# Kernel optimization log

Hardware: AMD Instinct MI355X
Metric: run time of the kernel (lower is better)

Reference implementation:

```python
import jax, jax.numpy as jnp
import numpy as np

D_MODEL = 1024
N_HEADS = 16
D_HEAD = D_MODEL // N_HEADS
SCALE = 1.0 / np.sqrt(D_HEAD)


def setup_inputs() -> dict:
    key = jax.random.key(0)
    ks = jax.random.split(key, 5)
    B, S = 2, 2048
    x = jax.random.normal(ks[0], (B, S, D_MODEL), dtype=jnp.float32)
    # torch F.linear weights have shape (d_out, d_in); kaiming-uniform-ish init
    bound = 1.0 / np.sqrt(D_MODEL)
    Wq = jax.random.uniform(ks[1], (D_MODEL, D_MODEL), jnp.float32, -bound, bound)
    Wk = jax.random.uniform(ks[2], (D_MODEL, D_MODEL), jnp.float32, -bound, bound)
    Wv = jax.random.uniform(ks[3], (D_MODEL, D_MODEL), jnp.float32, -bound, bound)
    Wo = jax.random.uniform(ks[4], (D_MODEL, D_MODEL), jnp.float32, -bound, bound)
    return {"x": x, "Wq": Wq, "Wk": Wk, "Wv": Wv, "Wo": Wo}


def reference(x, Wq, Wk, Wv, Wo):
    B, S, _ = x.shape
    # F.linear(x, W) = x @ W.T; reshape to [B, H, S, Dh]
    def proj(W):
        return (x @ W.T).reshape(B, S, N_HEADS, D_HEAD).transpose(0, 2, 1, 3)
    Q, K, V = proj(Wq), proj(Wk), proj(Wv)
    # scores [B, H, S, S]
    attn = jnp.einsum('bhqd,bhkd->bhqk', Q, K) * SCALE
    causal = jnp.tril(jnp.ones((S, S), dtype=bool))
    attn = jnp.where(causal, attn, -jnp.inf)
    attn = jax.nn.softmax(attn, axis=-1)
    out = jnp.einsum('bhqk,bhkd->bhqd', attn, V)
    out = out.transpose(0, 2, 1, 3).reshape(B, S, D_MODEL)
    return out @ Wo.T
```

## Files before the change

kernel.cpp:

```cpp
#include <hip/hip_runtime.h>


typedef __attribute__((ext_vector_type(8))) short short8;
typedef __attribute__((ext_vector_type(4))) float f32x4;
typedef __attribute__((ext_vector_type(4))) _Float16 half4;

#if __has_builtin(__builtin_amdgcn_exp2f)
#define EXP2F(x) __builtin_amdgcn_exp2f(x)
#else
#define EXP2F(x) exp2f(x)
#endif

__device__ __forceinline__ unsigned short f2bf(float f) {
  unsigned int x = __float_as_uint(f);
  x += 0x7fffu + ((x >> 16) & 1u);
  return (unsigned short)(x >> 16);
}

__device__ __forceinline__ void gload16(const void* g, void* l) {
  __builtin_amdgcn_global_load_lds(
      (const __attribute__((address_space(1))) void*)g,
      (__attribute__((address_space(3))) void*)l, 16, 0, 0);
}

__device__ __forceinline__ int swz64(int row, int sc) {
  return row * 64 + ((((sc >> 3) ^ (row & 7)) << 3) | (sc & 7));
}

__device__ __forceinline__ int swzG(int row, int chunk) {
  return row * 32 + (((chunk ^ ((row >> 1) & 3)) << 3));
}

__global__ void cast_kernel(const float* __restrict__ x, const float* __restrict__ wq,
                            const float* __restrict__ wk, const float* __restrict__ wv,
                            const float* __restrict__ wo,
                            unsigned short* __restrict__ xb, unsigned short* __restrict__ wqb,
                            unsigned short* __restrict__ wkb, unsigned short* __restrict__ wvb,
                            unsigned short* __restrict__ wob) {
  int id = blockIdx.x;
  const float* in; unsigned short* out; int blk; float sc = 1.f;
  if (id < 4096) { in = x; out = xb; blk = id; }
  else {
    int wsel = (id - 4096) >> 10;
    blk = (id - 4096) & 1023;
    switch (wsel) {
      case 0: in = wq; out = wqb; sc = 0.18033688011112042f; break;
      case 1: in = wk; out = wkb; break;
      case 2: in = wv; out = wvb; break;
      default: in = wo; out = wob; break;
    }
  }
  int i = blk * 256 + threadIdx.x;
  float4 v = ((const float4*)in)[i];
  union { unsigned short u[4]; uint2 p; } o;
  o.u[0] = f2bf(v.x * sc); o.u[1] = f2bf(v.y * sc);
  o.u[2] = f2bf(v.z * sc); o.u[3] = f2bf(v.w * sc);
  ((uint2*)out)[i] = o.p;
}

#define GK 1024

__global__ __launch_bounds__(256) void gemm_qkv_kernel(
    const unsigned short* __restrict__ X,
    const unsigned short* __restrict__ Wq,
    const unsigned short* __restrict__ Wk,
    const unsigned short* __restrict__ Wv,
    unsigned short* __restrict__ Qo,
    unsigned short* __restrict__ Ko,
    _Float16* __restrict__ Vt) {
  __shared__ unsigned short As[2][128 * 32];
  __shared__ unsigned short Bs[2][128 * 32];
  int id = blockIdx.x;
  int xcd = id & 7, j = id >> 3;
  int mb = j / 3;
  int nbT = xcd * 3 + (j - mb * 3);
  int sel = nbT >> 3, nb = nbT & 7;
  const unsigned short* W = sel == 0 ? Wq : (sel == 1 ? Wk : Wv);

  int tid = threadIdx.x;
  int w = tid >> 6, l = tid & 63, quad = l >> 4, lo = l & 15;
  int wm = (w >> 1) * 64, wn = (w & 1) * 64;

  int srow = tid >> 2;
  int slc = (tid & 3) ^ ((srow >> 1) & 3);
  int srow2 = (256 + tid) >> 2;
  int slc2 = (tid & 3) ^ ((srow2 >> 1) & 3);

  f32x4 acc[4][4];
#pragma unroll
  for (int i = 0; i < 4; i++)
#pragma unroll
    for (int jj = 0; jj < 4; jj++) acc[i][jj] = (f32x4){0.f, 0.f, 0.f, 0.f};

  gload16(X + (size_t)(mb * 128 + srow) * GK + slc * 8, (char*)As[0] + tid * 16);
  gload16(W + (size_t)(nb * 128 + srow) * GK + slc * 8, (char*)Bs[0] + tid * 16);
  gload16(X + (size_t)(mb * 128 + srow2) * GK + slc2 * 8, (char*)As[0] + (256 + tid) * 16);
  gload16(W + (size_t)(nb * 128 + srow2) * GK + slc2 * 8, (char*)Bs[0] + (256 + tid) * 16);

  for (int kt = 0; kt < 32; kt++) {
    __syncthreads();
    if (kt + 1 < 32) {
      int nb_ = (kt + 1) & 1, k0 = (kt + 1) * 32;
      gload16(X + (size_t)(mb * 128 + srow) * GK + k0 + slc * 8, (char*)As[nb_] + tid * 16);
      gload16(W + (size_t)(nb * 128 + srow) * GK + k0 + slc * 8, (char*)Bs[nb_] + tid * 16);
      gload16(X + (size_t)(mb * 128 + srow2) * GK + k0 + slc2 * 8,
              (char*)As[nb_] + (256 + tid) * 16);
      gload16(W + (size_t)(nb * 128 + srow2) * GK + k0 + slc2 * 8,
              (char*)Bs[nb_] + (256 + tid) * 16);
    }
    const unsigned short* as = As[kt & 1];
    const unsigned short* bs = Bs[kt & 1];
    short8 a[4], b[4];
#pragma unroll
    for (int mi = 0; mi < 4; mi++)
      a[mi] = *(const short8*)&as[swzG(wm + mi * 16 + lo, quad)];
#pragma unroll
    for (int ni = 0; ni < 4; ni++)
      b[ni] = *(const short8*)&bs[swzG(wn + ni * 16 + lo, quad)];
#pragma unroll
    for (int mi = 0; mi < 4; mi++)
#pragma unroll
      for (int ni = 0; ni < 4; ni++)
        acc[mi][ni] = __builtin_amdgcn_mfma_f32_16x16x32_bf16(a[mi], b[ni],
                                                              acc[mi][ni], 0, 0, 0);
  }
  if (sel == 2) {
#pragma unroll
    for (int mi = 0; mi < 4; mi++)
#pragma unroll
      for (int ni = 0; ni < 4; ni++) {
        int row0 = mb * 128 + wm + mi * 16 + quad * 4;
        int col = nb * 128 + wn + ni * 16 + lo;
        int bb = row0 >> 11, ss = row0 & 2047;
        int hh = col >> 6, dd = col & 63;
        half4 v;
#pragma unroll
        for (int r = 0; r < 4; r++) v[r] = (_Float16)acc[mi][ni][r];
        *(half4*)&Vt[((size_t)((bb * 16 + hh) * 64 + dd)) * 2048 + ss] = v;
      }
  } else {
    unsigned short* C = sel == 0 ? Qo : Ko;
#pragma unroll
    for (int mi = 0; mi < 4; mi++)
#pragma unroll
      for (int ni = 0; ni < 4; ni++)
#pragma unroll
        for (int r = 0; r < 4; r++) {
          int row = mb * 128 + wm + mi * 16 + quad * 4 + r;
          int col = nb * 128 + wn + ni * 16 + lo;
          C[(size_t)row * 1024 + col] = f2bf(acc[mi][ni][r]);
        }
  }
}

__global__ __launch_bounds__(256) void gemm_out_kernel(
    const unsigned short* __restrict__ A,
    const unsigned short* __restrict__ W,
    float* __restrict__ C) {
  __shared__ unsigned short As[2][128 * 32];
  __shared__ unsigned short Bs[2][64 * 32];
  int id = blockIdx.x;
  int nb = ((id & 7) << 1) | ((id >> 3) & 1);
  int mb = id >> 4;
  int tid = threadIdx.x;
  int w = tid >> 6, l = tid & 63, quad = l >> 4, lo = l & 15;
  int wm = w * 32;

  int srow = tid >> 2;
  int slc = (tid & 3) ^ ((srow >> 1) & 3);
  int srow2 = (256 + tid) >> 2;
  int slc2 = (tid & 3) ^ ((srow2 >> 1) & 3);

  f32x4 acc[2][4];
#pragma unroll
  for (int i = 0; i < 2; i++)
#pragma unroll
    for (int jj = 0; jj < 4; jj++) acc[i][jj] = (f32x4){0.f, 0.f, 0.f, 0.f};

  gload16(A + (size_t)(mb * 128 + srow) * GK + slc * 8, (char*)As[0] + tid * 16);
  gload16(A + (size_t)(mb * 128 + srow2) * GK + slc2 * 8, (char*)As[0] + (256 + tid) * 16);
  gload16(W + (size_t)(nb * 64 + srow) * GK + slc * 8, (char*)Bs[0] + tid * 16);

  for (int kt = 0; kt < 32; kt++) {
    __syncthreads();
    if (kt + 1 < 32) {
      int nb_ = (kt + 1) & 1, k0 = (kt + 1) * 32;
      gload16(A + (size_t)(mb * 128 + srow) * GK + k0 + slc * 8, (char*)As[nb_] + tid * 16);
      gload16(A + (size_t)(mb * 128 + srow2) * GK + k0 + slc2 * 8,
              (char*)As[nb_] + (256 + tid) * 16);
      gload16(W + (size_t)(nb * 64 + srow) * GK + k0 + slc * 8, (char*)Bs[nb_] + tid * 16);
    }
    const unsigned short* as = As[kt & 1];
    const unsigned short* bs = Bs[kt & 1];
    short8 a[2], b[4];
#pragma unroll
    for (int mi = 0; mi < 2; mi++)
      a[mi] = *(const short8*)&as[swzG(wm + mi * 16 + lo, quad)];
#pragma unroll
    for (int ni = 0; ni < 4; ni++)
      b[ni] = *(const short8*)&bs[swzG(ni * 16 + lo, quad)];
#pragma unroll
    for (int mi = 0; mi < 2; mi++)
#pragma unroll
      for (int ni = 0; ni < 4; ni++)
        acc[mi][ni] = __builtin_amdgcn_mfma_f32_16x16x32_bf16(a[mi], b[ni],
                                                              acc[mi][ni], 0, 0, 0);
  }
#pragma unroll
  for (int mi = 0; mi < 2; mi++)
#pragma unroll
    for (int ni = 0; ni < 4; ni++)
#pragma unroll
      for (int r = 0; r < 4; r++) {
        int row = mb * 128 + wm + mi * 16 + quad * 4 + r;
        int col = nb * 64 + ni * 16 + lo;
        C[(size_t)row * 1024 + col] = acc[mi][ni][r];
      }
}

__global__ __launch_bounds__(256, 4) void attn_kernel(
    const unsigned short* __restrict__ Q,
    const unsigned short* __restrict__ K,
    const _Float16* __restrict__ Vt,
    unsigned short* __restrict__ O) {
  const int S = 2048, DM = 1024;
  __shared__ unsigned short Ks[2][64 * 64];
  __shared__ _Float16 Vts[2][64 * 64];

  int id = blockIdx.x;
  int bh = ((id & 7) << 2) | ((id >> 3) & 3);
  int qt = 31 - (id >> 5);
  int b = bh >> 4, h = bh & 15;
  size_t base = (size_t)b * S * DM + h * 64;
  size_t baseVt = (size_t)(bh * 64) * S;

  int tid = threadIdx.x;
  int w = tid >> 6, lane = tid & 63, quad = lane >> 4, lo = lane & 15;
  int qrow0 = qt * 64 + w * 16;
  const half4 ones = {(_Float16)1.f, (_Float16)1.f, (_Float16)1.f, (_Float16)1.f};

  short8 qf[2];
#pragma unroll
  for (int d = 0; d < 2; d++)
    qf[d] = *(const short8*)(Q + base + (size_t)(qrow0 + lo) * DM + d * 32 + quad * 8);

#pragma unroll
  for (int jj = 0; jj < 2; jj++) {
    int s_ = jj * 256 + tid;
    int row = s_ >> 3, lc = (s_ & 7) ^ (row & 7);
    gload16(K + base + (size_t)row * DM + lc * 8, (char*)Ks[0] + s_ * 16);
    gload16(Vt + baseVt + (size_t)row * S + lc * 8, (char*)Vts[0] + s_ * 16);
  }

  f32x4 oacc[4], lacc;
  lacc = (f32x4){0.f, 0.f, 0.f, 0.f};
#pragma unroll
  for (int ni = 0; ni < 4; ni++) oacc[ni] = (f32x4){0.f, 0.f, 0.f, 0.f};

  int tend = qt + 1;
  for (int t = 0; t < tend; t++) {
    __syncthreads();
    if (t + 1 < tend) {
      int tb = (t + 1) & 1;
#pragma unroll
      for (int jj = 0; jj < 2; jj++) {
        int s_ = jj * 256 + tid;
        int row = s_ >> 3, lc = (s_ & 7) ^ (row & 7);
        gload16(K + base + (size_t)((t + 1) * 64 + row) * DM + lc * 8,
                (char*)Ks[tb] + s_ * 16);
        gload16(Vt + baseVt + (size_t)row * S + (t + 1) * 64 + lc * 8,
                (char*)Vts[tb] + s_ * 16);
      }
    }
    const unsigned short* ks = Ks[t & 1];
    const _Float16* vs = Vts[t & 1];

    f32x4 st[4];
#pragma unroll
    for (int kvt = 0; kvt < 4; kvt++) st[kvt] = (f32x4){0.f, 0.f, 0.f, 0.f};
#pragma unroll
    for (int kvt = 0; kvt < 4; kvt++)
#pragma unroll
      for (int d = 0; d < 2; d++) {
        short8 kf = *(const short8*)&ks[swz64(kvt * 16 + lo, d * 32 + quad * 8)];
        st[kvt] = __builtin_amdgcn_mfma_f32_16x16x32_bf16(kf, qf[d], st[kvt], 0, 0, 0);
      }

    if (t == tend - 1) {
      int qg = qrow0 + lo;
#pragma unroll
      for (int kvt = 0; kvt < 4; kvt++)
#pragma unroll
        for (int r = 0; r < 4; r++) {
          int kv = t * 64 + kvt * 16 + quad * 4 + r;
          if (kv > qg) st[kvt][r] = -1e30f;
        }
    }

    half4 pf[4];
#pragma unroll
    for (int kvt = 0; kvt < 4; kvt++) {
      half4 p4;
#pragma unroll
      for (int r = 0; r < 4; r++) p4[r] = (_Float16)EXP2F(st[kvt][r]);
      pf[kvt] = p4;
    }

#pragma unroll
    for (int kvt = 0; kvt < 4; kvt++) {
#pragma unroll
      for (int ni = 0; ni < 4; ni++) {
        half4 vf = *(const half4*)&vs[swz64(ni * 16 + lo, kvt * 16 + quad * 4)];
        oacc[ni] = __builtin_amdgcn_mfma_f32_16x16x16f16(pf[kvt], vf, oacc[ni], 0, 0, 0);
      }
      lacc = __builtin_amdgcn_mfma_f32_16x16x16f16(pf[kvt], ones, lacc, 0, 0, 0);
    }
  }

  float inv[4];
#pragma unroll
  for (int r = 0; r < 4; r++) inv[r] = 1.0f / lacc[r];
#pragma unroll
  for (int ni = 0; ni < 4; ni++)
#pragma unroll
    for (int r = 0; r < 4; r++) {
      int qg = qrow0 + quad * 4 + r;
      O[base + (size_t)qg * DM + ni * 16 + lo] = f2bf(oacc[ni][r] * inv[r]);
    }
}

extern "C" void kernel_launch(void* const* d_in, const int* in_sizes, int n_in,
                              void* d_out, int out_size, void* d_ws, size_t ws_size,
                              hipStream_t stream) {
  const float* x  = (const float*)d_in[0];
  const float* Wq = (const float*)d_in[1];
  const float* Wk = (const float*)d_in[2];
  const float* Wv = (const float*)d_in[3];
  const float* Wo = (const float*)d_in[4];
  float* out = (float*)d_out;
  char* ws = (char*)d_ws;

  unsigned short* Xb  = (unsigned short*)(ws);
  unsigned short* Wqb = (unsigned short*)(ws + (8ll  << 20));
  unsigned short* Wkb = (unsigned short*)(ws + (10ll << 20));
  unsigned short* Wvb = (unsigned short*)(ws + (12ll << 20));
  unsigned short* Wob = (unsigned short*)(ws + (14ll << 20));
  unsigned short* Qb  = (unsigned short*)(ws + (16ll << 20));
  unsigned short* Kb  = (unsigned short*)(ws + (24ll << 20));
  _Float16*       Vt  = (_Float16*)     (ws + (32ll << 20));
  unsigned short* Ob  = (unsigned short*)(ws + (40ll << 20));

  cast_kernel<<<8192, 256, 0, stream>>>(x, Wq, Wk, Wv, Wo, Xb, Wqb, Wkb, Wvb, Wob);
  gemm_qkv_kernel<<<768, 256, 0, stream>>>(Xb, Wqb, Wkb, Wvb, Qb, Kb, Vt);
  attn_kernel<<<1024, 256, 0, stream>>>(Qb, Kb, Vt, Ob);
  gemm_out_kernel<<<512, 256, 0, stream>>>(Ob, Wob, out);
}
```

Measured before the change: 182.1 us.

## Fuse all four stages into one persistent cooperative kernel with grid syncs

```diff
diff --git a/kernel.cpp b/kernel.cpp
--- a/kernel.cpp
+++ b/kernel.cpp
@@ -1,4 +1,7 @@
 #include <hip/hip_runtime.h>
+#include <hip/hip_cooperative_groups.h>
+
+namespace cg = cooperative_groups;
 
 
 typedef __attribute__((ext_vector_type(8))) short short8;
@@ -31,302 +34,294 @@
   return row * 32 + (((chunk ^ ((row >> 1) & 3)) << 3));
 }
 
-__global__ void cast_kernel(const float* __restrict__ x, const float* __restrict__ wq,
-                            const float* __restrict__ wk, const float* __restrict__ wv,
-                            const float* __restrict__ wo,
-                            unsigned short* __restrict__ xb, unsigned short* __restrict__ wqb,
-                            unsigned short* __restrict__ wkb, unsigned short* __restrict__ wvb,
-                            unsigned short* __restrict__ wob) {
-  int id = blockIdx.x;
-  const float* in; unsigned short* out; int blk; float sc = 1.f;
-  if (id < 4096) { in = x; out = xb; blk = id; }
-  else {
-    int wsel = (id - 4096) >> 10;
-    blk = (id - 4096) & 1023;
-    switch (wsel) {
-      case 0: in = wq; out = wqb; sc = 0.18033688011112042f; break;
-      case 1: in = wk; out = wkb; break;
-      case 2: in = wv; out = wvb; break;
-      default: in = wo; out = wob; break;
+__global__ __launch_bounds__(256, 3) void fused_kernel(
+    const float* __restrict__ x, const float* __restrict__ wq,
+    const float* __restrict__ wk, const float* __restrict__ wv,
+    const float* __restrict__ wo,
+    unsigned short* __restrict__ Xb, unsigned short* __restrict__ Wqb,
+    unsigned short* __restrict__ Wkb, unsigned short* __restrict__ Wvb,
+    unsigned short* __restrict__ Wob,
+    unsigned short* __restrict__ Qb, unsigned short* __restrict__ Kb,
+    _Float16* __restrict__ Vt, unsigned short* __restrict__ Ob,
+    float* __restrict__ out, int* __restrict__ ctr) {
+  cg::grid_group grid = cg::this_grid();
+  __shared__ __attribute__((aligned(16))) char smem[32768];
+  __shared__ int t_sh;
+  const int G = gridDim.x;
+  const int id = blockIdx.x, tid = threadIdx.x;
+  const int w = tid >> 6, lane = tid & 63, quad = lane >> 4, lo = lane & 15;
+  const int S = 2048, DM = 1024;
+
+  if (id == 0 && tid == 0) ctr[0] = 0;
+  for (long long j = (long long)id * 256 + tid; j < 2097152; j += (long long)G * 256) {
+    const float* in; unsigned short* outp; long long off; float sc = 1.f;
+    if (j < 1048576) { in = x; outp = Xb; off = j; }
+    else {
+      int wsel = (int)((j - 1048576) >> 18);
+      off = (j - 1048576) & 262143;
+      switch (wsel) {
+        case 0: in = wq; outp = Wqb; sc = 0.18033688011112042f; break;
+        case 1: in = wk; outp = Wkb; break;
+        case 2: in = wv; outp = Wvb; break;
+        default: in = wo; outp = Wob; break;
+      }
+    }
+    float4 v = ((const float4*)in)[off];
+    union { unsigned short u[4]; uint2 p; } o;
+    o.u[0] = f2bf(v.x * sc); o.u[1] = f2bf(v.y * sc);
+    o.u[2] = f2bf(v.z * sc); o.u[3] = f2bf(v.w * sc);
+    ((uint2*)outp)[off] = o.p;
+  }
+  __threadfence();
+  grid.sync();
+
+  {
+    unsigned short* As = (unsigned short*)smem;
+    unsigned short* Bs = (unsigned short*)(smem + 16384);
+    const int srow = tid >> 2, slc = (tid & 3) ^ ((srow >> 1) & 3);
+    const int srow2 = (256 + tid) >> 2, slc2 = (tid & 3) ^ ((srow2 >> 1) & 3);
+    const int wm = (w >> 1) * 64, wn = (w & 1) * 64;
+    for (int tile = id; tile < 768; tile += G) {
+      const int mb = tile & 31, nbT = tile >> 5;
+      const int sel = nbT >> 3, nb = nbT & 7;
+      const unsigned short* W = sel == 0 ? Wqb : (sel == 1 ? Wkb : Wvb);
+      const unsigned short* Xa  = Xb + (size_t)(mb * 128 + srow ) * 1024 + slc  * 8;
+      const unsigned short* Wa  = W  + (size_t)(nb * 128 + srow ) * 1024 + slc  * 8;
+      const unsigned short* Xa2 = Xb + (size_t)(mb * 128 + srow2) * 1024 + slc2 * 8;
+      const unsigned short* Wa2 = W  + (size_t)(nb * 128 + srow2) * 1024 + slc2 * 8;
+      __syncthreads();
+      gload16(Xa,  (char*)As + tid * 16);
+      gload16(Wa,  (char*)Bs + tid * 16);
+      gload16(Xa2, (char*)As + (256 + tid) * 16);
+      gload16(Wa2, (char*)Bs + (256 + tid) * 16);
+      f32x4 acc[4][4];
+#pragma unroll
+      for (int i = 0; i < 4; i++)
+#pragma unroll
+        for (int jj = 0; jj < 4; jj++) acc[i][jj] = (f32x4){0.f, 0.f, 0.f, 0.f};
+      for (int kt = 0; kt < 32; kt++) {
+        __syncthreads();
+        if (kt + 1 < 32) {
+          const int bo = ((kt + 1) & 1) * 4096, k0 = (kt + 1) * 32;
+          gload16(Xa + k0,  (char*)(As + bo) + tid * 16);
+          gload16(Wa + k0,  (char*)(Bs + bo) + tid * 16);
+          gload16(Xa2 + k0, (char*)(As + bo) + (256 + tid) * 16);
+          gload16(Wa2 + k0, (char*)(Bs + bo) + (256 + tid) * 16);
+        }
+        const unsigned short* as = As + (kt & 1) * 4096;
+        const unsigned short* bs = Bs + (kt & 1) * 4096;
+        short8 a[4], b[4];
+#pragma unroll
+        for (int mi = 0; mi < 4; mi++)
+          a[mi] = *(const short8*)&as[swzG(wm + mi * 16 + lo, quad)];
+#pragma unroll
+        for (int ni = 0; ni < 4; ni++)
+          b[ni] = *(const short8*)&bs[swzG(wn + ni * 16 + lo, quad)];
+#pragma unroll
+        for (int mi = 0; mi < 4; mi++)
+#pragma unroll
+          for (int ni = 0; ni < 4; ni++)
+            acc[mi][ni] = __builtin_amdgcn_mfma_f32_16x16x32_bf16(a[mi], b[ni],
+                                                                  acc[mi][ni], 0, 0, 0);
+      }
+      if (sel == 2) {
+#pragma unroll
+        for (int mi = 0; mi < 4; mi++)
+#pragma unroll
+          for (int ni = 0; ni < 4; ni++) {
+            int row0 = mb * 128 + wm + mi * 16 + quad * 4;
+            int col = nb * 128 + wn + ni * 16 + lo;
+            int bb = row0 >> 11, ss = row0 & 2047;
+            int hh = col >> 6, dd = col & 63;
+            half4 v;
+#pragma unroll
+            for (int r = 0; r < 4; r++) v[r] = (_Float16)acc[mi][ni][r];
+            *(half4*)&Vt[((size_t)((bb * 16 + hh) * 64 + dd)) * 2048 + ss] = v;
+          }
+      } else {
+        unsigned short* C = sel == 0 ? Qb : Kb;
+#pragma unroll
+        for (int mi = 0; mi < 4; mi++)
+#pragma unroll
+          for (int ni = 0; ni < 4; ni++)
+#pragma unroll
+            for (int r = 0; r < 4; r++) {
+              int row = mb * 128 + wm + mi * 16 + quad * 4 + r;
+              int col = nb * 128 + wn + ni * 16 + lo;
+              C[(size_t)row * 1024 + col] = f2bf(acc[mi][ni][r]);
+            }
+      }
     }
   }
-  int i = blk * 256 + threadIdx.x;
-  float4 v = ((const float4*)in)[i];
-  union { unsigned short u[4]; uint2 p; } o;
-  o.u[0] = f2bf(v.x * sc); o.u[1] = f2bf(v.y * sc);
-  o.u[2] = f2bf(v.z * sc); o.u[3] = f2bf(v.w * sc);
-  ((uint2*)out)[i] = o.p;
-}
-
-#define GK 1024
-
-__global__ __launch_bounds__(256) void gemm_qkv_kernel(
-    const unsigned short* __restrict__ X,
-    const unsigned short* __restrict__ Wq,
-    const unsigned short* __restrict__ Wk,
-    const unsigned short* __restrict__ Wv,
-    unsigned short* __restrict__ Qo,
-    unsigned short* __restrict__ Ko,
-    _Float16* __restrict__ Vt) {
-  __shared__ unsigned short As[2][128 * 32];
-  __shared__ unsigned short Bs[2][128 * 32];
-  int id = blockIdx.x;
-  int xcd = id & 7, j = id >> 3;
-  int mb = j / 3;
-  int nbT = xcd * 3 + (j - mb * 3);
-  int sel = nbT >> 3, nb = nbT & 7;
-  const unsigned short* W = sel == 0 ? Wq : (sel == 1 ? Wk : Wv);
-
-  int tid = threadIdx.x;
-  int w = tid >> 6, l = tid & 63, quad = l >> 4, lo = l & 15;
-  int wm = (w >> 1) * 64, wn = (w & 1) * 64;
-
-  int srow = tid >> 2;
-  int slc = (tid & 3) ^ ((srow >> 1) & 3);
-  int srow2 = (256 + tid) >> 2;
-  int slc2 = (tid & 3) ^ ((srow2 >> 1) & 3);
-
-  f32x4 acc[4][4];
-#pragma unroll
-  for (int i = 0; i < 4; i++)
-#pragma unroll
-    for (int jj = 0; jj < 4; jj++) acc[i][jj] = (f32x4){0.f, 0.f, 0.f, 0.f};
-
-  gload16(X + (size_t)(mb * 128 + srow) * GK + slc * 8, (char*)As[0] + tid * 16);
-  gload16(W + (size_t)(nb * 128 + srow) * GK + slc * 8, (char*)Bs[0] + tid * 16);
-  gload16(X + (size_t)(mb * 128 + srow2) * GK + slc2 * 8, (char*)As[0] + (256 + tid) * 16);
-  gload16(W + (size_t)(nb * 128 + srow2) * GK + slc2 * 8, (char*)Bs[0] + (256 + tid) * 16);
-
-  for (int kt = 0; kt < 32; kt++) {
-    __syncthreads();
-    if (kt + 1 < 32) {
-      int nb_ = (kt + 1) & 1, k0 = (kt + 1) * 32;
-      gload16(X + (size_t)(mb * 128 + srow) * GK + k0 + slc * 8, (char*)As[nb_] + tid * 16);
-      gload16(W + (size_t)(nb * 128 + srow) * GK + k0 + slc * 8, (char*)Bs[nb_] + tid * 16);
-      gload16(X + (size_t)(mb * 128 + srow2) * GK + k0 + slc2 * 8,
-              (char*)As[nb_] + (256 + tid) * 16);
-      gload16(W + (size_t)(nb * 128 + srow2) * GK + k0 + slc2 * 8,
-              (char*)Bs[nb_] + (256 + tid) * 16);
-    }
-    const unsigned short* as = As[kt & 1];
-    const unsigned short* bs = Bs[kt & 1];
-    short8 a[4], b[4];
-#pragma unroll
-    for (int mi = 0; mi < 4; mi++)
-      a[mi] = *(const short8*)&as[swzG(wm + mi * 16 + lo, quad)];
-#pragma unroll
-    for (int ni = 0; ni < 4; ni++)
-      b[ni] = *(const short8*)&bs[swzG(wn + ni * 16 + lo, quad)];
-#pragma unroll
-    for (int mi = 0; mi < 4; mi++)
-#pragma unroll
-      for (int ni = 0; ni < 4; ni++)
-        acc[mi][ni] = __builtin_amdgcn_mfma_f32_16x16x32_bf16(a[mi], b[ni],
-                                                              acc[mi][ni], 0, 0, 0);
-  }
-  if (sel == 2) {
-#pragma unroll
-    for (int mi = 0; mi < 4; mi++)
-#pragma unroll
-      for (int ni = 0; ni < 4; ni++) {
-        int row0 = mb * 128 + wm + mi * 16 + quad * 4;
-        int col = nb * 128 + wn + ni * 16 + lo;
-        int bb = row0 >> 11, ss = row0 & 2047;
-        int hh = col >> 6, dd = col & 63;
-        half4 v;
-#pragma unroll
-        for (int r = 0; r < 4; r++) v[r] = (_Float16)acc[mi][ni][r];
-        *(half4*)&Vt[((size_t)((bb * 16 + hh) * 64 + dd)) * 2048 + ss] = v;
-      }
-  } else {
-    unsigned short* C = sel == 0 ? Qo : Ko;
-#pragma unroll
-    for (int mi = 0; mi < 4; mi++)
-#pragma unroll
-      for (int ni = 0; ni < 4; ni++)
-#pragma unroll
-        for (int r = 0; r < 4; r++) {
-          int row = mb * 128 + wm + mi * 16 + quad * 4 + r;
-          int col = nb * 128 + wn + ni * 16 + lo;
-          C[(size_t)row * 1024 + col] = f2bf(acc[mi][ni][r]);
-        }
-  }
-}
-
-__global__ __launch_bounds__(256) void gemm_out_kernel(
-    const unsigned short* __restrict__ A,
-    const unsigned short* __restrict__ W,
-    float* __restrict__ C) {
-  __shared__ unsigned short As[2][128 * 32];
-  __shared__ unsigned short Bs[2][64 * 32];
-  int id = blockIdx.x;
-  int nb = ((id & 7) << 1) | ((id >> 3) & 1);
-  int mb = id >> 4;
-  int tid = threadIdx.x;
-  int w = tid >> 6, l = tid & 63, quad = l >> 4, lo = l & 15;
-  int wm = w * 32;
-
-  int srow = tid >> 2;
-  int slc = (tid & 3) ^ ((srow >> 1) & 3);
-  int srow2 = (256 + tid) >> 2;
-  int slc2 = (tid & 3) ^ ((srow2 >> 1) & 3);
-
-  f32x4 acc[2][4];
-#pragma unroll
-  for (int i = 0; i < 2; i++)
-#pragma unroll
-    for (int jj = 0; jj < 4; jj++) acc[i][jj] = (f32x4){0.f, 0.f, 0.f, 0.f};
-
-  gload16(A + (size_t)(mb * 128 + srow) * GK + slc * 8, (char*)As[0] + tid * 16);
-  gload16(A + (size_t)(mb * 128 + srow2) * GK + slc2 * 8, (char*)As[0] + (256 + tid) * 16);
-  gload16(W + (size_t)(nb * 64 + srow) * GK + slc * 8, (char*)Bs[0] + tid * 16);
-
-  for (int kt = 0; kt < 32; kt++) {
-    __syncthreads();
-    if (kt + 1 < 32) {
-      int nb_ = (kt + 1) & 1, k0 = (kt + 1) * 32;
-      gload16(A + (size_t)(mb * 128 + srow) * GK + k0 + slc * 8, (char*)As[nb_] + tid * 16);
-      gload16(A + (size_t)(mb * 128 + srow2) * GK + k0 + slc2 * 8,
-              (char*)As[nb_] + (256 + tid) * 16);
-      gload16(W + (size_t)(nb * 64 + srow) * GK + k0 + slc * 8, (char*)Bs[nb_] + tid * 16);
-    }
-    const unsigned short* as = As[kt & 1];
-    const unsigned short* bs = Bs[kt & 1];
-    short8 a[2], b[4];
-#pragma unroll
-    for (int mi = 0; mi < 2; mi++)
-      a[mi] = *(const short8*)&as[swzG(wm + mi * 16 + lo, quad)];
-#pragma unroll
-    for (int ni = 0; ni < 4; ni++)
-      b[ni] = *(const short8*)&bs[swzG(ni * 16 + lo, quad)];
-#pragma unroll
-    for (int mi = 0; mi < 2; mi++)
-#pragma unroll
-      for (int ni = 0; ni < 4; ni++)
-        acc[mi][ni] = __builtin_amdgcn_mfma_f32_16x16x32_bf16(a[mi], b[ni],
-                                                              acc[mi][ni], 0, 0, 0);
-  }
-#pragma unroll
-  for (int mi = 0; mi < 2; mi++)
-#pragma unroll
-    for (int ni = 0; ni < 4; ni++)
-#pragma unroll
-      for (int r = 0; r < 4; r++) {
-        int row = mb * 128 + wm + mi * 16 + quad * 4 + r;
-        int col = nb * 64 + ni * 16 + lo;
-        C[(size_t)row * 1024 + col] = acc[mi][ni][r];
-      }
-}
-
-__global__ __launch_bounds__(256, 4) void attn_kernel(
-    const unsigned short* __restrict__ Q,
-    const unsigned short* __restrict__ K,
-    const _Float16* __restrict__ Vt,
-    unsigned short* __restrict__ O) {
-  const int S = 2048, DM = 1024;
-  __shared__ unsigned short Ks[2][64 * 64];
-  __shared__ _Float16 Vts[2][64 * 64];
-
-  int id = blockIdx.x;
-  int bh = ((id & 7) << 2) | ((id >> 3) & 3);
-  int qt = 31 - (id >> 5);
-  int b = bh >> 4, h = bh & 15;
-  size_t base = (size_t)b * S * DM + h * 64;
-  size_t baseVt = (size_t)(bh * 64) * S;
-
-  int tid = threadIdx.x;
-  int w = tid >> 6, lane = tid & 63, quad = lane >> 4, lo = lane & 15;
-  int qrow0 = qt * 64 + w * 16;
-  const half4 ones = {(_Float16)1.f, (_Float16)1.f, (_Float16)1.f, (_Float16)1.f};
-
-  short8 qf[2];
-#pragma unroll
-  for (int d = 0; d < 2; d++)
-    qf[d] = *(const short8*)(Q + base + (size_t)(qrow0 + lo) * DM + d * 32 + quad * 8);
-
-#pragma unroll
-  for (int jj = 0; jj < 2; jj++) {
-    int s_ = jj * 256 + tid;
-    int row = s_ >> 3, lc = (s_ & 7) ^ (row & 7);
-    gload16(K + base + (size_t)row * DM + lc * 8, (char*)Ks[0] + s_ * 16);
-    gload16(Vt + baseVt + (size_t)row * S + lc * 8, (char*)Vts[0] + s_ * 16);
-  }
-
-  f32x4 oacc[4], lacc;
-  lacc = (f32x4){0.f, 0.f, 0.f, 0.f};
-#pragma unroll
-  for (int ni = 0; ni < 4; ni++) oacc[ni] = (f32x4){0.f, 0.f, 0.f, 0.f};
-
-  int tend = qt + 1;
-  for (int t = 0; t < tend; t++) {
-    __syncthreads();
-    if (t + 1 < tend) {
-      int tb = (t + 1) & 1;
+  __threadfence();
+  grid.sync();
+
+  {
+    unsigned short* Ks = (unsigned short*)smem;
+    _Float16* Vts = (_Float16*)(smem + 16384);
+    const half4 ones = {(_Float16)1.f, (_Float16)1.f, (_Float16)1.f, (_Float16)1.f};
+    while (true) {
+      __syncthreads();
+      if (tid == 0) t_sh = atomicAdd(ctr, 1);
+      __syncthreads();
+      const int tk = t_sh;
+      if (tk >= 1024) break;
+      const int qt = 31 - (tk >> 5), bh = tk & 31;
+      const int b = bh >> 4, h = bh & 15;
+      const size_t base = (size_t)b * S * DM + h * 64;
+      const size_t baseVt = (size_t)(bh * 64) * S;
+      const int qrow0 = qt * 64 + w * 16;
+
+      short8 qf[2];
+#pragma unroll
+      for (int d = 0; d < 2; d++)
+        qf[d] = *(const short8*)(Qb + base + (size_t)(qrow0 + lo) * DM + d * 32 + quad * 8);
+
 #pragma unroll
       for (int jj = 0; jj < 2; jj++) {
         int s_ = jj * 256 + tid;
         int row = s_ >> 3, lc = (s_ & 7) ^ (row & 7);
-        gload16(K + base + (size_t)((t + 1) * 64 + row) * DM + lc * 8,
-                (char*)Ks[tb] + s_ * 16);
-        gload16(Vt + baseVt + (size_t)row * S + (t + 1) * 64 + lc * 8,
-                (char*)Vts[tb] + s_ * 16);
-      }
-    }
-    const unsigned short* ks = Ks[t & 1];
-    const _Float16* vs = Vts[t & 1];
-
-    f32x4 st[4];
-#pragma unroll
-    for (int kvt = 0; kvt < 4; kvt++) st[kvt] = (f32x4){0.f, 0.f, 0.f, 0.f};
-#pragma unroll
-    for (int kvt = 0; kvt < 4; kvt++)
-#pragma unroll
-      for (int d = 0; d < 2; d++) {
-        short8 kf = *(const short8*)&ks[swz64(kvt * 16 + lo, d * 32 + quad * 8)];
-        st[kvt] = __builtin_amdgcn_mfma_f32_16x16x32_bf16(kf, qf[d], st[kvt], 0, 0, 0);
-      }
-
-    if (t == tend - 1) {
-      int qg = qrow0 + lo;
-#pragma unroll
-      for (int kvt = 0; kvt < 4; kvt++)
+        gload16(Kb + base + (size_t)row * DM + lc * 8, (char*)Ks + s_ * 16);
+        gload16(Vt + baseVt + (size_t)row * S + lc * 8, (char*)Vts + s_ * 16);
+      }
+
+      f32x4 oacc[4], lacc;
+      lacc = (f32x4){0.f, 0.f, 0.f, 0.f};
+#pragma unroll
+      for (int ni = 0; ni < 4; ni++) oacc[ni] = (f32x4){0.f, 0.f, 0.f, 0.f};
+
+      const int tend = qt + 1;
+      for (int tt = 0; tt < tend; tt++) {
+        __syncthreads();
+        if (tt + 1 < tend) {
+          const int tb = ((tt + 1) & 1) * 4096;
+#pragma unroll
+          for (int jj = 0; jj < 2; jj++) {
+            int s_ = jj * 256 + tid;
+            int row = s_ >> 3, lc = (s_ & 7) ^ (row & 7);
+            gload16(Kb + base + (size_t)((tt + 1) * 64 + row) * DM + lc * 8,
+                    (char*)(Ks + tb) + s_ * 16);
+            gload16(Vt + baseVt + (size_t)row * S + (tt + 1) * 64 + lc * 8,
+                    (char*)(Vts + tb) + s_ * 16);
+          }
+        }
+        const unsigned short* ks = Ks + (tt & 1) * 4096;
+        const _Float16* vs = Vts + (tt & 1) * 4096;
+
+        f32x4 st[4];
+#pragma unroll
+        for (int kvt = 0; kvt < 4; kvt++) st[kvt] = (f32x4){0.f, 0.f, 0.f, 0.f};
+#pragma unroll
+        for (int kvt = 0; kvt < 4; kvt++)
+#pragma unroll
+          for (int d = 0; d < 2; d++) {
+            short8 kf = *(const short8*)&ks[swz64(kvt * 16 + lo, d * 32 + quad * 8)];
+            st[kvt] = __builtin_amdgcn_mfma_f32_16x16x32_bf16(kf, qf[d], st[kvt], 0, 0, 0);
+          }
+
+        if (tt == tend - 1) {
+          int qg = qrow0 + lo;
+#pragma unroll
+          for (int kvt = 0; kvt < 4; kvt++)
+#pragma unroll
+            for (int r = 0; r < 4; r++) {
+              int kv = tt * 64 + kvt * 16 + quad * 4 + r;
+              if (kv > qg) st[kvt][r] = -1e30f;
+            }
+        }
+
+        half4 pf[4];
+#pragma unroll
+        for (int kvt = 0; kvt < 4; kvt++) {
+          half4 p4;
+#pragma unroll
+          for (int r = 0; r < 4; r++) p4[r] = (_Float16)EXP2F(st[kvt][r]);
+          pf[kvt] = p4;
+        }
+
+#pragma unroll
+        for (int kvt = 0; kvt < 4; kvt++) {
+#pragma unroll
+          for (int ni = 0; ni < 4; ni++) {
+            half4 vf = *(const half4*)&vs[swz64(ni * 16 + lo, kvt * 16 + quad * 4)];
+            oacc[ni] = __builtin_amdgcn_mfma_f32_16x16x16f16(pf[kvt], vf, oacc[ni], 0, 0, 0);
+          }
+          lacc = __builtin_amdgcn_mfma_f32_16x16x16f16(pf[kvt], ones, lacc, 0, 0, 0);
+        }
+      }
+
+      float inv[4];
+#pragma unroll
+      for (int r = 0; r < 4; r++) inv[r] = 1.0f / lacc[r];
+#pragma unroll
+      for (int ni = 0; ni < 4; ni++)
 #pragma unroll
         for (int r = 0; r < 4; r++) {
-          int kv = t * 64 + kvt * 16 + quad * 4 + r;
-          if (kv > qg) st[kvt][r] = -1e30f;
-        }
-    }
-
-    half4 pf[4];
-#pragma unroll
-    for (int kvt = 0; kvt < 4; kvt++) {
-      half4 p4;
-#pragma unroll
-      for (int r = 0; r < 4; r++) p4[r] = (_Float16)EXP2F(st[kvt][r]);
-      pf[kvt] = p4;
-    }
-
-#pragma unroll
-    for (int kvt = 0; kvt < 4; kvt++) {
-#pragma unroll
-      for (int ni = 0; ni < 4; ni++) {
-        half4 vf = *(const half4*)&vs[swz64(ni * 16 + lo, kvt * 16 + quad * 4)];
-        oacc[ni] = __builtin_amdgcn_mfma_f32_16x16x16f16(pf[kvt], vf, oacc[ni], 0, 0, 0);
-      }
-      lacc = __builtin_amdgcn_mfma_f32_16x16x16f16(pf[kvt], ones, lacc, 0, 0, 0);
+          int qg = qrow0 + quad * 4 + r;
+          Ob[base + (size_t)qg * DM + ni * 16 + lo] = f2bf(oacc[ni][r] * inv[r]);
+        }
     }
   }
-
-  float inv[4];
-#pragma unroll
-  for (int r = 0; r < 4; r++) inv[r] = 1.0f / lacc[r];
-#pragma unroll
-  for (int ni = 0; ni < 4; ni++)
-#pragma unroll
-    for (int r = 0; r < 4; r++) {
-      int qg = qrow0 + quad * 4 + r;
-      O[base + (size_t)qg * DM + ni * 16 + lo] = f2bf(oacc[ni][r] * inv[r]);
+  __threadfence();
+  grid.sync();
+
+  {
+    unsigned short* As = (unsigned short*)smem;
+    unsigned short* Bs = (unsigned short*)(smem + 16384);
+    const int srow = tid >> 2, slc = (tid & 3) ^ ((srow >> 1) & 3);
+    const int srow2 = (256 + tid) >> 2, slc2 = (tid & 3) ^ ((srow2 >> 1) & 3);
+    const int wm = w * 32;
+    for (int tile = id; tile < 512; tile += G) {
+      const int mb = tile >> 4, nb = tile & 15;
+      const unsigned short* Aa  = Ob + (size_t)(mb * 128 + srow ) * 1024 + slc  * 8;
+      const unsigned short* Aa2 = Ob + (size_t)(mb * 128 + srow2) * 1024 + slc2 * 8;
+      const unsigned short* Wa  = Wob + (size_t)(nb * 64 + srow) * 1024 + slc * 8;
+      __syncthreads();
+      gload16(Aa,  (char*)As + tid * 16);
+      gload16(Aa2, (char*)As + (256 + tid) * 16);
+      gload16(Wa,  (char*)Bs + tid * 16);
+      f32x4 acc[2][4];
+#pragma unroll
+      for (int i = 0; i < 2; i++)
+#pragma unroll
+        for (int jj = 0; jj < 4; jj++) acc[i][jj] = (f32x4){0.f, 0.f, 0.f, 0.f};
+      for (int kt = 0; kt < 32; kt++) {
+        __syncthreads();
+        if (kt + 1 < 32) {
+          const int k0 = (kt + 1) * 32;
+          const int boA = ((kt + 1) & 1) * 4096, boB = ((kt + 1) & 1) * 2048;
+          gload16(Aa + k0,  (char*)(As + boA) + tid * 16);
+          gload16(Aa2 + k0, (char*)(As + boA) + (256 + tid) * 16);
+          gload16(Wa + k0,  (char*)(Bs + boB) + tid * 16);
+        }
+        const unsigned short* as = As + (kt & 1) * 4096;
+        const unsigned short* bs = Bs + (kt & 1) * 2048;
+        short8 a[2], b[4];
+#pragma unroll
+        for (int mi = 0; mi < 2; mi++)
+          a[mi] = *(const short8*)&as[swzG(wm + mi * 16 + lo, quad)];
+#pragma unroll
+        for (int ni = 0; ni < 4; ni++)
+          b[ni] = *(const short8*)&bs[swzG(ni * 16 + lo, quad)];
+#pragma unroll
+        for (int mi = 0; mi < 2; mi++)
+#pragma unroll
+          for (int ni = 0; ni < 4; ni++)
+            acc[mi][ni] = __builtin_amdgcn_mfma_f32_16x16x32_bf16(a[mi], b[ni],
+                                                                  acc[mi][ni], 0, 0, 0);
+      }
+#pragma unroll
+      for (int mi = 0; mi < 2; mi++)
+#pragma unroll
+        for (int ni = 0; ni < 4; ni++)
+#pragma unroll
+          for (int r = 0; r < 4; r++) {
+            int row = mb * 128 + wm + mi * 16 + quad * 4 + r;
+            int col = nb * 64 + ni * 16 + lo;
+            out[(size_t)row * 1024 + col] = acc[mi][ni][r];
+          }
     }
+  }
 }
 
 extern "C" void kernel_launch(void* const* d_in, const int* in_sizes, int n_in,
@@ -349,9 +344,17 @@
   unsigned short* Kb  = (unsigned short*)(ws + (24ll << 20));
   _Float16*       Vt  = (_Float16*)     (ws + (32ll << 20));
   unsigned short* Ob  = (unsigned short*)(ws + (40ll << 20));
-
-  cast_kernel<<<8192, 256, 0, stream>>>(x, Wq, Wk, Wv, Wo, Xb, Wqb, Wkb, Wvb, Wob);
-  gemm_qkv_kernel<<<768, 256, 0, stream>>>(Xb, Wqb, Wkb, Wvb, Qb, Kb, Vt);
-  attn_kernel<<<1024, 256, 0, stream>>>(Qb, Kb, Vt, Ob);
-  gemm_out_kernel<<<512, 256, 0, stream>>>(Ob, Wob, out);
-}
+  int*            ctr = (int*)           (ws + (48ll << 20));
+
+  int bpc = 0;
+  (void)hipOccupancyMaxActiveBlocksPerMultiprocessor(&bpc, fused_kernel, 256, 0);
+  if (bpc < 1) bpc = 1;
+  int G = bpc * 256;
+  if (G > 768) G = 768;
+
+  void* args[] = {(void*)&x, (void*)&Wq, (void*)&Wk, (void*)&Wv, (void*)&Wo,
+                  (void*)&Xb, (void*)&Wqb, (void*)&Wkb, (void*)&Wvb, (void*)&Wob,
+                  (void*)&Qb, (void*)&Kb, (void*)&Vt, (void*)&Ob,
+                  (void*)&out, (void*)&ctr};
+  hipLaunchCooperativeKernel((void*)fused_kernel, dim3(G), dim3(256), args, 0, stream);
+}
```

Result: slower. 425.1 us (+133.4%).
